# Kernel tuning notes

Measured on AMD Instinct MI355X. Metric: run time of the kernel, lower is better.

Reference implementation:

```python
import jax, jax.numpy as jnp
import numpy as np

B, C, H, W, NH = 8, 256, 32, 32, 4  # batch, channels, height, width, heads


def groupnorm(x, w, b, eps=1e-5):
    # GroupNorm with 1 group: normalize over (C,H,W) per sample
    mu = x.mean(axis=(1, 2, 3), keepdims=True)
    var = x.var(axis=(1, 2, 3), keepdims=True)
    xn = (x - mu) * jax.lax.rsqrt(var + eps)
    return xn * w[None, :, None, None] + b[None, :, None, None]


def setup_inputs() -> dict:
    key = jax.random.key(0)
    ks = jax.random.split(key, 6)
    C4 = 4 * C
    s = lambda k, shape, scale: jax.random.normal(k, shape, jnp.float32) * scale
    return {
        "x": jax.random.normal(ks[0], (B, C, H, W), jnp.float32),
        "qkv_w": s(ks[1], (3 * C, C), 0.05),   # 1x1 conv, no bias
        "uh_w": s(ks[2], (C, C), 0.05),
        "uh_b": jnp.zeros((C,), jnp.float32),
        "n1_w": jnp.ones((C,), jnp.float32),
        "n1_b": jnp.zeros((C,), jnp.float32),
        "n2_w": jnp.ones((C,), jnp.float32),
        "n2_b": jnp.zeros((C,), jnp.float32),
        "f1_w": s(ks[3], (C4, C), 0.05),
        "f1_b": jnp.zeros((C4,), jnp.float32),
        "f2_w": s(ks[4], (C, C4), 0.05),
        "f2_b": jnp.zeros((C,), jnp.float32),
        # torch inits these to 0; use nonzero values so both branches contribute
        "gamma_attn": jnp.array(0.5, jnp.float32),
        "gamma_ffn": jnp.array(0.5, jnp.float32),
    }


def reference(x, qkv_w, uh_w, uh_b, n1_w, n1_b, n2_w, n2_b,
              f1_w, f1_b, f2_w, f2_b, gamma_attn, gamma_ffn):
    Bx, Cx, Hx, Wx = x.shape
    N = Hx * Wx
    dk = Cx // NH
    # --- attention branch (eval mode: DropPath is identity) ---
    xn = groupnorm(x, n1_w, n1_b).reshape(Bx, Cx, N)
    qkv = jnp.einsum('oc,bcn->bon', qkv_w, xn)          # 1x1 conv == channel matmul
    q, k, v = [t.reshape(Bx, NH, dk, N) for t in jnp.split(qkv, 3, axis=1)]
    scores = jnp.einsum('bhdi,bhdj->bhij', q, k) / np.float32(np.sqrt(dk))
    attn = jax.nn.softmax(scores, axis=-1)               # [B,H,N,N]
    out = jnp.einsum('bhij,bhdj->bhdi', attn, v).reshape(Bx, Cx, N)
    uh = jnp.einsum('oc,bcn->bon', uh_w, out) + uh_b[None, :, None]
    x2 = x + gamma_attn * uh.reshape(Bx, Cx, Hx, Wx)
    # --- FFN branch ---
    h = groupnorm(x2, n2_w, n2_b).reshape(Bx, Cx, N)
    h = jax.nn.silu(jnp.einsum('oc,bcn->bon', f1_w, h) + f1_b[None, :, None])
    h = jnp.einsum('oc,bcn->bon', f2_w, h) + f2_b[None, :, None]
    return x2 + gamma_ffn * h.reshape(Bx, Cx, Hx, Wx)
```

## Files before the change

kernel.cpp:

```cpp
#include <hip/hip_runtime.h>
#include <math.h>

#define Bsz 8
#define Cch 256
#define Nsp 1024
#define NHd 4
#define QS  0.18033688011112042f

using bf16x8  = __attribute__((ext_vector_type(8))) short;
using f32x4   = __attribute__((ext_vector_type(4))) float;
using ushort8 = __attribute__((ext_vector_type(8))) unsigned short;
#define MFMA(a,b,c) __builtin_amdgcn_mfma_f32_16x16x32_bf16(a,b,c,0,0,0)

__device__ inline unsigned short f2bf(float f) {
    unsigned int u = __float_as_uint(f);
    u = u + 0x7fffu + ((u >> 16) & 1u);
    return (unsigned short)(u >> 16);
}
__device__ inline float bf2f(unsigned short u) {
    return __uint_as_float((unsigned int)u << 16);
}
__device__ inline unsigned int cvtpk(float lo, float hi) {
    unsigned int r;
    asm("v_cvt_pk_bf16_f32 %0, %1, %2" : "=v"(r) : "v"(lo), "v"(hi));
    return r;
}

__global__ __launch_bounds__(256) void wconv_gn(const float* __restrict__ a, const float* __restrict__ b,
                                                const float* __restrict__ c, const float* __restrict__ d,
                                                unsigned short* __restrict__ o,
                                                const float* __restrict__ x,
                                                float* __restrict__ part) {
    if (blockIdx.x < 3072) {
        size_t i = (size_t)blockIdx.x * 256 + threadIdx.x;
        float v;
        if (i < 196608) v = a[i];
        else if (i < 262144) v = b[i - 196608];
        else if (i < 524288) v = c[i - 262144];
        else v = d[i - 524288];
        o[i] = f2bf(v);
        return;
    }
    int blk = blockIdx.x - 3072;
    int bb = blk >> 6;
    const float* xb = x + (size_t)bb * (Cch * Nsp) + (size_t)(blk & 63) * 4096;
    int t = threadIdx.x;
    float s = 0.f, s2 = 0.f;
    for (int i = t; i < 4096; i += 256) { float v = xb[i]; s += v; s2 += v * v; }
    __shared__ float sh[256], sh2[256];
    sh[t] = s; sh2[t] = s2; __syncthreads();
    for (int off = 128; off; off >>= 1) {
        if (t < off) { sh[t] += sh[t + off]; sh2[t] += sh2[t + off]; }
        __syncthreads();
    }
    if (t == 0) { part[blk * 2] = sh[0]; part[blk * 2 + 1] = sh2[0]; }
}

template<int K, int KL, int NFRAG>
__global__ __launch_bounds__(256, 4) void gemm_lds(
        const unsigned short* __restrict__ W,
        const unsigned short* __restrict__ Xcl,
        int epi, int act, int xmode,
        unsigned short* __restrict__ ocl, int Ocl, int ocol0,
        unsigned short* __restrict__ orm,
        float* __restrict__ pf, const float* __restrict__ res,
        unsigned short* __restrict__ x2cl,
        const float* __restrict__ gamma, const float* __restrict__ bias,
        float* __restrict__ part,
        const float* __restrict__ gnpart,
        const float* __restrict__ gnw, const float* __restrict__ gnb) {
    static_assert(KL == 256 && K == 256, "single-round K only");
    constexpr int NTILE = NFRAG * 16;
    constexpr int CPR = KL / 8;
    constexpr int TOTCH = NTILE * CPR;
    int b = blockIdx.z, nb = blockIdx.x, ob = blockIdx.y;
    int t = threadIdx.x, w = t >> 6, l = t & 63, lg = l >> 4, lm = l & 15;
    __shared__ unsigned short Xs[NTILE * KL];
    __shared__ float sgn[2];
    const unsigned short* Xb = Xcl + ((size_t)b * Nsp + nb * NTILE) * K;
    int o_base = ob * 256 + w * 64;
    const unsigned short* Wp = W + (size_t)(o_base + lm) * K + 8 * lg;
    int m8 = lm & 7;

    bf16x8 wA0, wA1, wA2, wA3, wB0, wB1, wB2, wB3, wC0, wC1, wC2, wC3;
    #define WL(d0, d1, d2, d3, ks_) do {                                   \
        d0 = *(const bf16x8*)(Wp + (size_t)(0)      + (ks_) * 32);         \
        d1 = *(const bf16x8*)(Wp + (size_t)16 * K   + (ks_) * 32);         \
        d2 = *(const bf16x8*)(Wp + (size_t)32 * K   + (ks_) * 32);         \
        d3 = *(const bf16x8*)(Wp + (size_t)48 * K   + (ks_) * 32);         \
    } while (0)
    WL(wA0, wA1, wA2, wA3, 0);
    WL(wB0, wB1, wB2, wB3, 1);

    if (xmode == 0) {
        #pragma unroll
        for (int i = 0; i < TOTCH / 256; i++) {
            int c = i * 256 + t;
            int n = c / CPR, s = c % CPR;
            int gc = s ^ (n & 7);
            *(bf16x8*)&Xs[c * 8] = *(const bf16x8*)(Xb + (size_t)n * K + gc * 8);
        }
    } else if (xmode == 1) {
        if (t < 64) {
            float s = gnpart[(b * 64 + t) * 2], s2 = gnpart[(b * 64 + t) * 2 + 1];
            for (int m = 1; m < 64; m <<= 1) { s += __shfl_xor(s, m); s2 += __shfl_xor(s2, m); }
            if (t == 0) {
                float inv_n = 1.f / (Cch * Nsp);
                float mu = s * inv_n;
                float var = s2 * inv_n - mu * mu;
                sgn[0] = mu; sgn[1] = rsqrtf(var + 1e-5f);
            }
        }
        __syncthreads();
        float mu = sgn[0], rs = sgn[1];
        #pragma unroll
        for (int i = 0; i < TOTCH / 256; i++) {
            int c = i * 256 + t;
            int n = c / CPR, s = c % CPR;
            int gc = s ^ (n & 7);
            ushort8 xv = *(const ushort8*)(Xb + (size_t)n * K + gc * 8);
            f32x4 w0 = *(const f32x4*)(gnw + gc * 8);
            f32x4 w1 = *(const f32x4*)(gnw + gc * 8 + 4);
            f32x4 b0 = *(const f32x4*)(gnb + gc * 8);
            f32x4 b1 = *(const f32x4*)(gnb + gc * 8 + 4);
            ushort8 rr;
            #pragma unroll
            for (int j = 0; j < 4; j++) {
                rr[j]     = f2bf((bf2f(xv[j])     - mu) * rs * w0[j] + b0[j]);
                rr[4 + j] = f2bf((bf2f(xv[4 + j]) - mu) * rs * w1[j] + b1[j]);
            }
            *(ushort8*)&Xs[c * 8] = rr;
        }
    } else if (xmode == 2) {
        const size_t SPO = (size_t)Bsz * Nsp * Cch;
        #pragma unroll
        for (int i = 0; i < TOTCH / 256; i++) {
            int c = i * 256 + t;
            int n = c / CPR, s = c % CPR;
            int gc = s ^ (n & 7);
            const unsigned short* p0 = Xb + (size_t)n * K + gc * 8;
            int h = gc >> 3;
            int gn = nb * NTILE + n;
            float a0[8] = {};
            float lsum = 0.f;
            #pragma unroll
            for (int sp = 0; sp < 4; sp++) {
                ushort8 ov = *(const ushort8*)(p0 + (size_t)sp * SPO);
                #pragma unroll
                for (int j = 0; j < 8; j++) a0[j] += bf2f(ov[j]);
                lsum += gnpart[(((size_t)sp * Bsz + b) * NHd + h) * Nsp + gn];
            }
            float inv = 1.f / lsum;
            ushort8 rr;
            #pragma unroll
            for (int j = 0; j < 8; j++) rr[j] = f2bf(a0[j] * inv);
            *(ushort8*)&Xs[c * 8] = rr;
        }
    } else {
        if (t < 64) {
            float s = gnpart[(b * 64 + t) * 2], s2 = gnpart[(b * 64 + t) * 2 + 1];
            for (int m = 1; m < 64; m <<= 1) { s += __shfl_xor(s, m); s2 += __shfl_xor(s2, m); }
            if (t == 0) {
                float inv_n = 1.f / (Cch * Nsp);
                float mu = s * inv_n;
                float var = s2 * inv_n - mu * mu;
                sgn[0] = mu; sgn[1] = rsqrtf(var + 1e-5f);
            }
        }
        __syncthreads();
        float mu = sgn[0], rs = sgn[1];
        int n = t & 31;
        #pragma unroll
        for (int i = 0; i < 4; i++) {
            int G = i * 8 + (t >> 5);
            const float* xr = res + ((size_t)b * Cch + G * 8) * Nsp + (size_t)nb * NTILE + n;
            ushort8 rr;
            #pragma unroll
            for (int j = 0; j < 8; j++) {
                float val = xr[(size_t)j * Nsp];
                rr[j] = f2bf((val - mu) * rs * gnw[G * 8 + j] + gnb[G * 8 + j]);
            }
            int slot = G ^ (n & 7);
            *(ushort8*)&Xs[(n * 32 + slot) * 8] = rr;
        }
    }
    __syncthreads();

    f32x4 acc[4][NFRAG] = {};
    #define KS(w0_, w1_, w2_, w3_, ks_) do {                               \
        _Pragma("unroll")                                                  \
        for (int nf = 0; nf < NFRAG; nf++) {                               \
            int slot = ((ks_) * 4 + lg) ^ m8;                              \
            bf16x8 xf = *(const bf16x8*)&Xs[((nf * 16 + lm) * CPR + slot) * 8]; \
            acc[0][nf] = MFMA(w0_, xf, acc[0][nf]);                        \
            acc[1][nf] = MFMA(w1_, xf, acc[1][nf]);                        \
            acc[2][nf] = MFMA(w2_, xf, acc[2][nf]);                        \
            acc[3][nf] = MFMA(w3_, xf, acc[3][nf]);                        \
        }                                                                  \
    } while (0)
    WL(wC0, wC1, wC2, wC3, 2); KS(wA0, wA1, wA2, wA3, 0);
    WL(wA0, wA1, wA2, wA3, 3); KS(wB0, wB1, wB2, wB3, 1);
    WL(wB0, wB1, wB2, wB3, 4); KS(wC0, wC1, wC2, wC3, 2);
    WL(wC0, wC1, wC2, wC3, 5); KS(wA0, wA1, wA2, wA3, 3);
    WL(wA0, wA1, wA2, wA3, 6); KS(wB0, wB1, wB2, wB3, 4);
    WL(wB0, wB1, wB2, wB3, 7); KS(wC0, wC1, wC2, wC3, 5);
    KS(wA0, wA1, wA2, wA3, 6);
    KS(wB0, wB1, wB2, wB3, 7);
    #undef WL
    #undef KS

    if (epi == 0) {
        if (act == 3 && o_base >= 512) {
            #pragma unroll
            for (int nf = 0; nf < NFRAG; nf++) {
                int n = nb * NTILE + nf * 16 + lm;
                #pragma unroll
                for (int q = 0; q < 4; q++)
                    #pragma unroll
                    for (int r = 0; r < 4; r++) {
                        int o = o_base + q * 16 + 4 * lg + r - 512;
                        orm[((size_t)b * Cch + o) * Nsp + n] = f2bf(acc[q][nf][r]);
                    }
            }
        } else {
            float sc = (act == 3 && o_base < 256) ? QS : 1.f;
            #pragma unroll
            for (int nf = 0; nf < NFRAG; nf++) {
                int n = nb * NTILE + nf * 16 + lm;
                unsigned short* dst = ocl + ((size_t)b * Nsp + n) * Ocl + ocol0 + o_base + 4 * lg;
                #pragma unroll
                for (int q = 0; q < 4; q++) {
                    unsigned long long pk = 0;
                    #pragma unroll
                    for (int r = 0; r < 4; r++) {
                        int o = o_base + q * 16 + 4 * lg + r;
                        float v = acc[q][nf][r];
                        if (bias) v += bias[o];
                        if (act == 1) v = v / (1.f + __expf(-v));
                        else v *= sc;
                        pk |= (unsigned long long)f2bf(v) << (16 * r);
                    }
                    *(unsigned long long*)(dst + q * 16) = pk;
                }
            }
        }
    } else {
        float g = gamma[0];
        float ps = 0.f, ps2 = 0.f;
        #pragma unroll
        for (int nf = 0; nf < NFRAG; nf++) {
            int n = nb * NTILE + nf * 16 + lm;
            unsigned short* cdst = x2cl + ((size_t)b * Nsp + n) * Cch + o_base + 4 * lg;
            #pragma unroll
            for (int q = 0; q < 4; q++) {
                unsigned long long pk = 0;
                #pragma unroll
                for (int r = 0; r < 4; r++) {
                    int o = o_base + q * 16 + 4 * lg + r;
                    float v = acc[q][nf][r];
                    if (bias) v += bias[o];
                    size_t idx = ((size_t)b * Cch + o) * Nsp + n;
                    float ov = res[idx] + g * v;
                    pf[idx] = ov;
                    ps += ov; ps2 += ov * ov;
                    pk |= (unsigned long long)f2bf(ov) << (16 * r);
                }
                *(unsigned long long*)(cdst + q * 16) = pk;
            }
        }
        float* rsh  = (float*)&Xs[0];
        float* rsh2 = rsh + 256;
        __syncthreads();
        rsh[t] = ps; rsh2[t] = ps2; __syncthreads();
        for (int off = 128; off; off >>= 1) {
            if (t < off) { rsh[t] += rsh[t + off]; rsh2[t] += rsh2[t + off]; }
            __syncthreads();
        }
        if (t == 0) {
            int slot = b * gridDim.x + nb;
            part[slot * 2] = rsh[0]; part[slot * 2 + 1] = rsh2[0];
        }
    }
}

__global__ __launch_bounds__(1024, 2) void ffn_fused(
        const unsigned short* __restrict__ Wf1,
        const unsigned short* __restrict__ Wf2,
        const unsigned short* __restrict__ x2cl,
        const float* __restrict__ gnpart,
        const float* __restrict__ gnw, const float* __restrict__ gnb,
        const float* __restrict__ f1b, const float* __restrict__ f2b,
        const float* __restrict__ gamma,
        const float* __restrict__ x2, float* __restrict__ out) {
    int b = blockIdx.z, nb = blockIdx.x;
    int t = threadIdx.x, w = t >> 6, l = t & 63, lg = l >> 4, lm = l & 15;
    __shared__ unsigned short Xs[32 * 256];
    __shared__ unsigned short H[4][32 * 256];
    __shared__ float sgn[2];
    const unsigned short* Xb = x2cl + ((size_t)b * Nsp + nb * 32) * 256;
    int m8 = lm & 7;

    bf16x8 wA0, wA1, wA2, wA3, wB0, wB1, wB2, wB3, wC0, wC1, wC2, wC3;
    const unsigned short* Wp = Wf1 + (size_t)(w * 64 + lm) * 256 + 8 * lg;
    #define WL1(d0, d1, d2, d3, ks_) do {                                  \
        d0 = *(const bf16x8*)(Wp + (ks_) * 32);                            \
        d1 = *(const bf16x8*)(Wp + (size_t)16 * 256 + (ks_) * 32);         \
        d2 = *(const bf16x8*)(Wp + (size_t)32 * 256 + (ks_) * 32);         \
        d3 = *(const bf16x8*)(Wp + (size_t)48 * 256 + (ks_) * 32);         \
    } while (0)

    if (t < 64) {
        float s = gnpart[(b * 64 + t) * 2], s2 = gnpart[(b * 64 + t) * 2 + 1];
        for (int m = 1; m < 64; m <<= 1) { s += __shfl_xor(s, m); s2 += __shfl_xor(s2, m); }
        if (t == 0) {
            float inv_n = 1.f / (Cch * Nsp);
            float mu = s * inv_n;
            float var = s2 * inv_n - mu * mu;
            sgn[0] = mu; sgn[1] = rsqrtf(var + 1e-5f);
        }
    }
    WL1(wA0, wA1, wA2, wA3, 0);
    WL1(wB0, wB1, wB2, wB3, 1);
    __syncthreads();
    {
        float mu = sgn[0], rs = sgn[1];
        int c = t;
        int n = c >> 5, s = c & 31;
        int gc = s ^ (n & 7);
        ushort8 xv = *(const ushort8*)(Xb + (size_t)n * 256 + gc * 8);
        f32x4 w0 = *(const f32x4*)(gnw + gc * 8);
        f32x4 w1 = *(const f32x4*)(gnw + gc * 8 + 4);
        f32x4 b0 = *(const f32x4*)(gnb + gc * 8);
        f32x4 b1 = *(const f32x4*)(gnb + gc * 8 + 4);
        ushort8 rr;
        #pragma unroll
        for (int j = 0; j < 4; j++) {
            rr[j]     = f2bf((bf2f(xv[j])     - mu) * rs * w0[j] + b0[j]);
            rr[4 + j] = f2bf((bf2f(xv[4 + j]) - mu) * rs * w1[j] + b1[j]);
        }
        *(ushort8*)&Xs[c * 8] = rr;
    }
    __syncthreads();

    f32x4 acc[4][2];
    #pragma unroll
    for (int q = 0; q < 4; q++)
        #pragma unroll
        for (int nf = 0; nf < 2; nf++) acc[q][nf] = (f32x4){0.f, 0.f, 0.f, 0.f};
    #define KS1(w0_, w1_, w2_, w3_, ks_) do {                              \
        _Pragma("unroll")                                                  \
        for (int nf = 0; nf < 2; nf++) {                                   \
            int slot = ((ks_) * 4 + lg) ^ m8;                              \
            bf16x8 xf = *(const bf16x8*)&Xs[((nf * 16 + lm) * 32 + slot) * 8]; \
            acc[0][nf] = MFMA(w0_, xf, acc[0][nf]);                        \
            acc[1][nf] = MFMA(w1_, xf, acc[1][nf]);                        \
            acc[2][nf] = MFMA(w2_, xf, acc[2][nf]);                        \
            acc[3][nf] = MFMA(w3_, xf, acc[3][nf]);                        \
        }                                                                  \
    } while (0)
    WL1(wC0, wC1, wC2, wC3, 2); KS1(wA0, wA1, wA2, wA3, 0);
    WL1(wA0, wA1, wA2, wA3, 3); KS1(wB0, wB1, wB2, wB3, 1);
    WL1(wB0, wB1, wB2, wB3, 4); KS1(wC0, wC1, wC2, wC3, 2);
    WL1(wC0, wC1, wC2, wC3, 5); KS1(wA0, wA1, wA2, wA3, 3);
    WL1(wA0, wA1, wA2, wA3, 6); KS1(wB0, wB1, wB2, wB3, 4);
    WL1(wB0, wB1, wB2, wB3, 7); KS1(wC0, wC1, wC2, wC3, 5);
    KS1(wA0, wA1, wA2, wA3, 6);
    KS1(wB0, wB1, wB2, wB3, 7);
    #undef WL1
    #undef KS1

    const unsigned short* Wp2 = Wf2 + (size_t)(w * 16 + lm) * 1024 + 8 * lg;
    bf16x8 fa, fb, fc, fd, fe, ff, fg, fh;
    #define WL2(d0, ks_) d0 = *(const bf16x8*)(Wp2 + (ks_) * 32)
    WL2(fa, 0); WL2(fb, 1); WL2(fc, 2); WL2(fd, 3); WL2(fe, 4); WL2(ff, 5);

    {
        int hb = w >> 2;
        #pragma unroll
        for (int nf = 0; nf < 2; nf++) {
            int n = nf * 16 + lm;
            #pragma unroll
            for (int q = 0; q < 4; q++) {
                unsigned long long pk = 0;
                #pragma unroll
                for (int r = 0; r < 4; r++) {
                    int o1 = w * 64 + q * 16 + 4 * lg + r;
                    float v = acc[q][nf][r] + f1b[o1];
                    v = v / (1.f + __expf(-v));
                    pk |= (unsigned long long)f2bf(v) << (16 * r);
                }
                int G = (w & 3) * 8 + q * 2 + (lg >> 1);
                int slot = G ^ (n & 7);
                *(unsigned long long*)&H[hb][(n * 32 + slot) * 8 + 4 * (lg & 1)] = pk;
            }
        }
    }
    __syncthreads();

    f32x4 ac2[2] = {};
    #define KS2(e0, g_) do {                                               \
        int slot = (((g_) & 7) * 4 + lg) ^ m8;                             \
        const unsigned short* Hp = H[(g_) >> 3];                           \
        _Pragma("unroll")                                                  \
        for (int nf = 0; nf < 2; nf++) {                                   \
            bf16x8 xf = *(const bf16x8*)&Hp[((nf * 16 + lm) * 32 + slot) * 8]; \
            ac2[nf] = MFMA(e0, xf, ac2[nf]);                               \
        }                                                                  \
    } while (0)
    WL2(fg, 6);  KS2(fa, 0);
    WL2(fh, 7);  KS2(fb, 1);
    WL2(fa, 8);  KS2(fc, 2);
    WL2(fb, 9);  KS2(fd, 3);
    WL2(fc, 10); KS2(fe, 4);
    WL2(fd, 11); KS2(ff, 5);
    WL2(fe, 12); KS2(fg, 6);
    WL2(ff, 13); KS2(fh, 7);
    WL2(fg, 14); KS2(fa, 8);
    WL2(fh, 15); KS2(fb, 9);
    WL2(fa, 16); KS2(fc, 10);
    WL2(fb, 17); KS2(fd, 11);
    WL2(fc, 18); KS2(fe, 12);
    WL2(fd, 19); KS2(ff, 13);
    WL2(fe, 20); KS2(fg, 14);
    WL2(ff, 21); KS2(fh, 15);
    WL2(fg, 22); KS2(fa, 16);
    WL2(fh, 23); KS2(fb, 17);
    WL2(fa, 24); KS2(fc, 18);
    WL2(fb, 25); KS2(fd, 19);
    WL2(fc, 26); KS2(fe, 20);
    WL2(fd, 27); KS2(ff, 21);
    WL2(fe, 28); KS2(fg, 22);
    WL2(ff, 29); KS2(fh, 23);
    WL2(fg, 30); KS2(fa, 24);
    WL2(fh, 31); KS2(fb, 25);
    KS2(fc, 26);
    KS2(fd, 27);
    KS2(fe, 28);
    KS2(ff, 29);
    KS2(fg, 30);
    KS2(fh, 31);
    #undef WL2
    #undef KS2

    float gm = gamma[0];
    #pragma unroll
    for (int nf = 0; nf < 2; nf++) {
        int n = nb * 32 + nf * 16 + lm;
        #pragma unroll
        for (int r = 0; r < 4; r++) {
            int o = w * 16 + 4 * lg + r;
            size_t idx = ((size_t)b * Cch + o) * Nsp + n;
            out[idx] = x2[idx] + gm * (ac2[nf][r] + f2b[o]);
        }
    }
}

__global__ __launch_bounds__(256) void attn_mfma8(const unsigned short* __restrict__ qk,
                                                  const unsigned short* __restrict__ v,
                                                  unsigned short* __restrict__ Opart,
                                                  float* __restrict__ lpart) {
    int L = blockIdx.x;
    int xcd = L & 7, jj = L >> 3;
    int g = xcd * 4 + (jj >> 5);
    int m = jj & 31;
    int h = g & 3, b = g >> 2;
    int ib = m & 7, sp = m >> 3;
    int t = threadIdx.x, w = t >> 6, l = t & 63, lg = l >> 4, lm = l & 15;
    __shared__ unsigned short KVs[2][4096];
    __shared__ unsigned short P[4][2][32][36];
    int i0 = ib * 128 + w * 32;
    int j0 = sp * 256;
    const unsigned short* qb = qk + ((size_t)b * Nsp + i0 + lm) * 512 + h * 64 + 8 * lg;
    bf16x8 qf00 = *(const bf16x8*)(qb);
    bf16x8 qf01 = *(const bf16x8*)(qb + 32);
    bf16x8 qf10 = *(const bf16x8*)(qb + 16 * 512);
    bf16x8 qf11 = *(const bf16x8*)(qb + 16 * 512 + 32);

    const unsigned short *gs0, *gs1;
    int lo0, lo1;
    size_t gstep;
    if (t < 128) {
        int c = 2 * t;
        int r = c >> 3, s = c & 7, swr = r & 7;
        const unsigned short* rowp = qk + ((size_t)b * Nsp + j0 + r) * 512 + 256 + h * 64;
        gs0 = rowp + ((s ^ swr) * 8);
        gs1 = rowp + (((s + 1) ^ swr) * 8);
        lo0 = c * 8; lo1 = lo0 + 8;
        gstep = (size_t)32 * 512;
    } else {
        int c = 2 * (t - 128);
        int d = c >> 2, s = c & 3, swd = d & 3;
        const unsigned short* rowp = v + ((size_t)b * Cch + h * 64 + d) * Nsp + j0;
        gs0 = rowp + ((s ^ swd) * 8);
        gs1 = rowp + (((s + 1) ^ swd) * 8);
        lo0 = 2048 + c * 8; lo1 = lo0 + 8;
        gstep = 32;
    }
    int cA = (lg ^ (lm & 7)) * 8;
    int cB = ((4 + lg) ^ (lm & 7)) * 8;
    int cV = (lg ^ (lm & 3)) * 8;

    f32x4 O00 = {}, O01 = {}, O02 = {}, O03 = {};
    f32x4 O10 = {}, O11 = {}, O12 = {}, O13 = {};
    float ls0 = 0.f, ls1 = 0.f;
    bf16x8 sg0, sg1;

    #define ISSUE(tile) do { sg0 = *(const bf16x8*)(gs0 + (size_t)(tile) * gstep); \
                             sg1 = *(const bf16x8*)(gs1 + (size_t)(tile) * gstep); } while (0)
    #define WRITE(bu) do { *(bf16x8*)&KVs[bu][lo0] = sg0; \
                           *(bf16x8*)&KVs[bu][lo1] = sg1; } while (0)
    #define QKC8(bu, pb) do {                                                     \
        const unsigned short* Ka = KVs[bu] + lm * 64;                             \
        const unsigned short* Kc = KVs[bu] + (16 + lm) * 64;                      \
        bf16x8 k00 = *(const bf16x8*)(Ka + cA);                                   \
        bf16x8 k01 = *(const bf16x8*)(Ka + cB);                                   \
        bf16x8 k10 = *(const bf16x8*)(Kc + cA);                                   \
        bf16x8 k11 = *(const bf16x8*)(Kc + cB);                                   \
        f32x4 s00 = {}, s01 = {}, s10 = {}, s11 = {};                             \
        s00 = MFMA(k00, qf00, s00); s00 = MFMA(k01, qf01, s00);                   \
        s01 = MFMA(k00, qf10, s01); s01 = MFMA(k01, qf11, s01);                   \
        s10 = MFMA(k10, qf00, s10); s10 = MFMA(k11, qf01, s10);                   \
        s11 = MFMA(k10, qf10, s11); s11 = MFMA(k11, qf11, s11);                   \
        float p0, p1, p2, p3; uint2 pk;                                           \
        p0 = exp2f(s00[0]); p1 = exp2f(s00[1]); p2 = exp2f(s00[2]); p3 = exp2f(s00[3]); \
        ls0 += (p0 + p1) + (p2 + p3);                                             \
        pk.x = cvtpk(p0, p1); pk.y = cvtpk(p2, p3);                               \
        *(uint2*)&P[w][pb][lm][4 * lg] = pk;                                      \
        p0 = exp2f(s01[0]); p1 = exp2f(s01[1]); p2 = exp2f(s01[2]); p3 = exp2f(s01[3]); \
        ls1 += (p0 + p1) + (p2 + p3);                                             \
        pk.x = cvtpk(p0, p1); pk.y = cvtpk(p2, p3);                               \
        *(uint2*)&P[w][pb][16 + lm][4 * lg] = pk;                                 \
        p0 = exp2f(s10[0]); p1 = exp2f(s10[1]); p2 = exp2f(s10[2]); p3 = exp2f(s10[3]); \
        ls0 += (p0 + p1) + (p2 + p3);                                             \
        pk.x = cvtpk(p0, p1); pk.y = cvtpk(p2, p3);                               \
        *(uint2*)&P[w][pb][lm][16 + 4 * lg] = pk;                                 \
        p0 = exp2f(s11[0]); p1 = exp2f(s11[1]); p2 = exp2f(s11[2]); p3 = exp2f(s11[3]); \
        ls1 += (p0 + p1) + (p2 + p3);                                             \
        pk.x = cvtpk(p0, p1); pk.y = cvtpk(p2, p3);                               \
        *(uint2*)&P[w][pb][16 + lm][16 + 4 * lg] = pk;                            \
    } while (0)
    #define PVC8(bu, pb) do {                                                     \
        bf16x8 pa0 = *(const bf16x8*)&P[w][pb][lm][8 * lg];                       \
        bf16x8 pa1 = *(const bf16x8*)&P[w][pb][16 + lm][8 * lg];                  \
        const unsigned short* Vl = KVs[bu] + 2048;                                \
        bf16x8 v0 = *(const bf16x8*)(Vl + lm * 32 + cV);                          \
        bf16x8 v1 = *(const bf16x8*)(Vl + (16 + lm) * 32 + cV);                   \
        bf16x8 v2 = *(const bf16x8*)(Vl + (32 + lm) * 32 + cV);                   \
        bf16x8 v3 = *(const bf16x8*)(Vl + (48 + lm) * 32 + cV);                   \
        O00 = MFMA(v0, pa0, O00); O10 = MFMA(v0, pa1, O10);                       \
        O01 = MFMA(v1, pa0, O01); O11 = MFMA(v1, pa1, O11);                       \
        O02 = MFMA(v2, pa0, O02); O12 = MFMA(v2, pa1, O12);                       \
        O03 = MFMA(v3, pa0, O03); O13 = MFMA(v3, pa1, O13);                       \
    } while (0)

    ISSUE(0); WRITE(0); __syncthreads();
    ISSUE(1);
    QKC8(0, 0);
    __syncthreads();
    WRITE(1);
    __syncthreads();
    #pragma unroll
    for (int tt = 1; tt < 8; tt++) {
        if (tt < 7) ISSUE(tt + 1);
        QKC8(tt & 1, tt & 1);
        PVC8((tt - 1) & 1, (tt - 1) & 1);
        __syncthreads();
        if (tt < 7) WRITE((tt + 1) & 1);
        __syncthreads();
    }
    PVC8(1, 1);
    #undef ISSUE
    #undef WRITE
    #undef QKC8
    #undef PVC8

    ls0 += __shfl_xor(ls0, 16); ls0 += __shfl_xor(ls0, 32);
    ls1 += __shfl_xor(ls1, 16); ls1 += __shfl_xor(ls1, 32);
    if (lg == 0) {
        float* lp = lpart + (((size_t)sp * Bsz + b) * NHd + h) * Nsp + i0 + lm;
        lp[0] = ls0;
        lp[16] = ls1;
    }
    unsigned short* ob0 = Opart + (((size_t)sp * Bsz + b) * Nsp + i0 + lm) * Cch + h * 64 + 4 * lg;
    unsigned short* ob1 = ob0 + (size_t)16 * Cch;
    uint2 pk;
    #define STO(dt, Oa, Ob_) \
        pk.x = cvtpk(Oa[0], Oa[1]); pk.y = cvtpk(Oa[2], Oa[3]); \
        *(uint2*)(ob0 + dt * 16) = pk; \
        pk.x = cvtpk(Ob_[0], Ob_[1]); pk.y = cvtpk(Ob_[2], Ob_[3]); \
        *(uint2*)(ob1 + dt * 16) = pk;
    STO(0, O00, O10) STO(1, O01, O11) STO(2, O02, O12) STO(3, O03, O13)
    #undef STO
}

extern "C" void kernel_launch(void* const* d_in, const int* in_sizes, int n_in,
                              void* d_out, int out_size, void* d_ws, size_t ws_size,
                              hipStream_t stream) {
    const float* x      = (const float*)d_in[0];
    const float* qkv_w  = (const float*)d_in[1];
    const float* uh_w   = (const float*)d_in[2];
    const float* uh_b   = (const float*)d_in[3];
    const float* n1_w   = (const float*)d_in[4];
    const float* n1_b   = (const float*)d_in[5];
    const float* n2_w   = (const float*)d_in[6];
    const float* n2_b   = (const float*)d_in[7];
    const float* f1_w   = (const float*)d_in[8];
    const float* f1_b   = (const float*)d_in[9];
    const float* f2_w   = (const float*)d_in[10];
    const float* f2_b   = (const float*)d_in[11];
    const float* g_attn = (const float*)d_in[12];
    const float* g_ffn  = (const float*)d_in[13];
    float* out = (float*)d_out;
    char* ws = (char*)d_ws;

    float*          part1   = (float*)(ws + 1024);
    float*          part2   = (float*)(ws + 5120);
    unsigned short* wbf     = (unsigned short*)(ws + 16384);
    float*          lpart   = (float*)(ws + 2097152);
    unsigned short* qk_cl   = (unsigned short*)(ws + 6291456);
    unsigned short* vbuf    = (unsigned short*)(ws + 14680064);
    unsigned short* x2cl    = (unsigned short*)(ws + 14680064);
    unsigned short* Opart   = (unsigned short*)(ws + 23068672);
    float*          x2      = (float*)(ws + 50331648);

    unsigned short* wbf_qkv = wbf;
    unsigned short* wbf_uh  = wbf + 196608;
    unsigned short* wbf_f1  = wbf + 262144;
    unsigned short* wbf_f2  = wbf + 524288;

    wconv_gn<<<3584, 256, 0, stream>>>(qkv_w, uh_w, f1_w, f2_w, wbf, x, part1);

    gemm_lds<256, 256, 2><<<dim3(32, 3, Bsz), 256, 0, stream>>>(wbf_qkv,
        (const unsigned short*)x, 0, 3, 3,
        qk_cl, 512, 0, vbuf, nullptr, x, nullptr, nullptr, nullptr, nullptr,
        part1, n1_w, n1_b);
    attn_mfma8<<<1024, 256, 0, stream>>>(qk_cl, vbuf, Opart, lpart);
    gemm_lds<256, 256, 1><<<dim3(64, 1, Bsz), 256, 0, stream>>>(wbf_uh, Opart, 2, 0, 2,
        nullptr, 0, 0, nullptr, x2, x, x2cl, g_attn, uh_b, part2,
        lpart, nullptr, nullptr);

    ffn_fused<<<dim3(32, 1, Bsz), 1024, 0, stream>>>(wbf_f1, wbf_f2, x2cl,
        part2, n2_w, n2_b, f1_b, f2_b, g_ffn, x2, out);
}
```

Baseline: 105.9 us.

## Triple-buffer attention K/V tiles and store x2 residual as bf16

The attention kernel moves from double to triple buffering of K/V tiles in LDS and uses a single P buffer per wave. This drops one of the two barriers per tile iteration, and PV now runs before QK within each step. Separately, the x2 residual passed from the uh GEMM to the FFN kernel is stored as bf16 instead of fp32, which halves that write and read traffic. The cost is lower precision in the residual added to the final output, plus more LDS per attention block.

New measurement: 106.6 us. About the same (+0.7%).

```diff
diff --git a/kernel.cpp b/kernel.cpp
--- a/kernel.cpp
+++ b/kernel.cpp
@@ -261,7 +261,7 @@
                     if (bias) v += bias[o];
                     size_t idx = ((size_t)b * Cch + o) * Nsp + n;
                     float ov = res[idx] + g * v;
-                    pf[idx] = ov;
+                    orm[idx] = f2bf(ov);
                     ps += ov; ps2 += ov * ov;
                     pk |= (unsigned long long)f2bf(ov) << (16 * r);
                 }
@@ -291,7 +291,7 @@
         const float* __restrict__ gnw, const float* __restrict__ gnb,
         const float* __restrict__ f1b, const float* __restrict__ f2b,
         const float* __restrict__ gamma,
-        const float* __restrict__ x2, float* __restrict__ out) {
+        const unsigned short* __restrict__ x2, float* __restrict__ out) {
     int b = blockIdx.z, nb = blockIdx.x;
     int t = threadIdx.x, w = t >> 6, l = t & 63, lg = l >> 4, lm = l & 15;
     __shared__ unsigned short Xs[32 * 256];
@@ -450,7 +450,7 @@
         for (int r = 0; r < 4; r++) {
             int o = w * 16 + 4 * lg + r;
             size_t idx = ((size_t)b * Cch + o) * Nsp + n;
-            out[idx] = x2[idx] + gm * (ac2[nf][r] + f2b[o]);
+            out[idx] = bf2f(x2[idx]) + gm * (ac2[nf][r] + f2b[o]);
         }
     }
 }
@@ -466,8 +466,8 @@
     int h = g & 3, b = g >> 2;
     int ib = m & 7, sp = m >> 3;
     int t = threadIdx.x, w = t >> 6, l = t & 63, lg = l >> 4, lm = l & 15;
-    __shared__ unsigned short KVs[2][4096];
-    __shared__ unsigned short P[4][2][32][36];
+    __shared__ unsigned short KVs[3][4096];
+    __shared__ unsigned short P[4][32][36];
     int i0 = ib * 128 + w * 32;
     int j0 = sp * 256;
     const unsigned short* qb = qk + ((size_t)b * Nsp + i0 + lm) * 512 + h * 64 + 8 * lg;
@@ -509,7 +509,7 @@
                              sg1 = *(const bf16x8*)(gs1 + (size_t)(tile) * gstep); } while (0)
     #define WRITE(bu) do { *(bf16x8*)&KVs[bu][lo0] = sg0; \
                            *(bf16x8*)&KVs[bu][lo1] = sg1; } while (0)
-    #define QKC8(bu, pb) do {                                                     \
+    #define QKC8(bu) do {                                                         \
         const unsigned short* Ka = KVs[bu] + lm * 64;                             \
         const unsigned short* Kc = KVs[bu] + (16 + lm) * 64;                      \
         bf16x8 k00 = *(const bf16x8*)(Ka + cA);                                   \
@@ -525,23 +525,23 @@
         p0 = exp2f(s00[0]); p1 = exp2f(s00[1]); p2 = exp2f(s00[2]); p3 = exp2f(s00[3]); \
         ls0 += (p0 + p1) + (p2 + p3);                                             \
         pk.x = cvtpk(p0, p1); pk.y = cvtpk(p2, p3);                               \
-        *(uint2*)&P[w][pb][lm][4 * lg] = pk;                                      \
+        *(uint2*)&P[w][lm][4 * lg] = pk;                                          \
         p0 = exp2f(s01[0]); p1 = exp2f(s01[1]); p2 = exp2f(s01[2]); p3 = exp2f(s01[3]); \
         ls1 += (p0 + p1) + (p2 + p3);                                             \
         pk.x = cvtpk(p0, p1); pk.y = cvtpk(p2, p3);                               \
-        *(uint2*)&P[w][pb][16 + lm][4 * lg] = pk;                                 \
+        *(uint2*)&P[w][16 + lm][4 * lg] = pk;                                     \
         p0 = exp2f(s10[0]); p1 = exp2f(s10[1]); p2 = exp2f(s10[2]); p3 = exp2f(s10[3]); \
         ls0 += (p0 + p1) + (p2 + p3);                                             \
         pk.x = cvtpk(p0, p1); pk.y = cvtpk(p2, p3);                               \
-        *(uint2*)&P[w][pb][lm][16 + 4 * lg] = pk;                                 \
+        *(uint2*)&P[w][lm][16 + 4 * lg] = pk;                                     \
         p0 = exp2f(s11[0]); p1 = exp2f(s11[1]); p2 = exp2f(s11[2]); p3 = exp2f(s11[3]); \
         ls1 += (p0 + p1) + (p2 + p3);                                             \
         pk.x = cvtpk(p0, p1); pk.y = cvtpk(p2, p3);                               \
-        *(uint2*)&P[w][pb][16 + lm][16 + 4 * lg] = pk;                            \
+        *(uint2*)&P[w][16 + lm][16 + 4 * lg] = pk;                                \
     } while (0)
-    #define PVC8(bu, pb) do {                                                     \
-        bf16x8 pa0 = *(const bf16x8*)&P[w][pb][lm][8 * lg];                       \
-        bf16x8 pa1 = *(const bf16x8*)&P[w][pb][16 + lm][8 * lg];                  \
+    #define PVC8(bu) do {                                                         \
+        bf16x8 pa0 = *(const bf16x8*)&P[w][lm][8 * lg];                           \
+        bf16x8 pa1 = *(const bf16x8*)&P[w][16 + lm][8 * lg];                      \
         const unsigned short* Vl = KVs[bu] + 2048;                                \
         bf16x8 v0 = *(const bf16x8*)(Vl + lm * 32 + cV);                          \
         bf16x8 v1 = *(const bf16x8*)(Vl + (16 + lm) * 32 + cV);                   \
@@ -555,20 +555,18 @@
 
     ISSUE(0); WRITE(0); __syncthreads();
     ISSUE(1);
-    QKC8(0, 0);
-    __syncthreads();
+    QKC8(0);
     WRITE(1);
     __syncthreads();
     #pragma unroll
     for (int tt = 1; tt < 8; tt++) {
         if (tt < 7) ISSUE(tt + 1);
-        QKC8(tt & 1, tt & 1);
-        PVC8((tt - 1) & 1, (tt - 1) & 1);
+        PVC8((tt - 1) % 3);
+        QKC8(tt % 3);
+        if (tt < 7) WRITE((tt + 1) % 3);
         __syncthreads();
-        if (tt < 7) WRITE((tt + 1) & 1);
-        __syncthreads();
-    }
-    PVC8(1, 1);
+    }
+    PVC8(1);
     #undef ISSUE
     #undef WRITE
     #undef QKC8
@@ -621,7 +619,7 @@
     unsigned short* vbuf    = (unsigned short*)(ws + 14680064);
     unsigned short* x2cl    = (unsigned short*)(ws + 14680064);
     unsigned short* Opart   = (unsigned short*)(ws + 23068672);
-    float*          x2      = (float*)(ws + 50331648);
+    unsigned short* x2rm    = (unsigned short*)(ws + 50331648);
 
     unsigned short* wbf_qkv = wbf;
     unsigned short* wbf_uh  = wbf + 196608;
@@ -636,9 +634,9 @@
         part1, n1_w, n1_b);
     attn_mfma8<<<1024, 256, 0, stream>>>(qk_cl, vbuf, Opart, lpart);
     gemm_lds<256, 256, 1><<<dim3(64, 1, Bsz), 256, 0, stream>>>(wbf_uh, Opart, 2, 0, 2,
-        nullptr, 0, 0, nullptr, x2, x, x2cl, g_attn, uh_b, part2,
+        nullptr, 0, 0, x2rm, nullptr, x, x2cl, g_attn, uh_b, part2,
         lpart, nullptr, nullptr);
 
     ffn_fused<<<dim3(32, 1, Bsz), 1024, 0, stream>>>(wbf_f1, wbf_f2, x2cl,
-        part2, n2_w, n2_b, f1_b, f2_b, g_ffn, x2, out);
-}
+        part2, n2_w, n2_b, f1_b, f2_b, g_ffn, x2rm, out);
+}
```
